# Optimization experiments

Hardware: AMD Instinct MI355X
Metric: run time of the kernel (lower is better)

The kernel has to match this reference:

```python
import jax, jax.numpy as jnp
import numpy as np

H, D, Kd, Vd = 16, 1024, 64, 64
N, Mlen = 4096, 4096


def setup_inputs() -> dict:
    key = jax.random.key(0)
    ks = jax.random.split(key, 7)
    X = jax.random.normal(ks[0], (N, D), dtype=jnp.float32)
    M = jax.random.normal(ks[1], (Mlen, D), dtype=jnp.float32)
    mask = jax.random.randint(ks[2], (N, Mlen), 0, 2, dtype=jnp.int32)
    Wq = jax.random.normal(ks[3], (H, D, Kd), dtype=jnp.float32)
    Wk = jax.random.normal(ks[4], (H, D, Kd), dtype=jnp.float32)
    Wv = jax.random.normal(ks[5], (H, D, Vd), dtype=jnp.float32)
    Wo = jax.random.normal(ks[6], (H, Vd, D), dtype=jnp.float32)
    return {"X": X, "M": M, "mask": mask, "Wq": Wq, "Wk": Wk, "Wv": Wv, "Wo": Wo}


def reference(X, M, mask, Wq, Wk, Wv, Wo):
    # Projections: [h,n,k], [h,m,k], [h,m,v]
    Q = jnp.einsum('nd,hdk->hnk', X, Wq)
    K = jnp.einsum('md,hdk->hmk', M, Wk)
    V = jnp.einsum('md,hdv->hmv', M, Wv)
    # Masked attention (no scaling, matching the source)
    logits = jnp.einsum('hnk,hmk->hnm', Q, K)
    logits = jnp.where(mask[None, :, :] == 0, -jnp.inf, logits)
    weights = jax.nn.softmax(logits, axis=-1)
    O = jnp.einsum('hnm,hmv->hnv', weights, V)
    Y = jnp.einsum('hnv,hvd->nd', O, Wo)
    return Y
```

## Files before the change

kernel.cpp:

```cpp
#include <hip/hip_runtime.h>

typedef _Float16 half8 __attribute__((ext_vector_type(8)));
typedef _Float16 half4 __attribute__((ext_vector_type(4)));
typedef __fp16 fp16x2 __attribute__((ext_vector_type(2)));
typedef short short8 __attribute__((ext_vector_type(8)));
typedef short short4v __attribute__((ext_vector_type(4)));
typedef float floatx4 __attribute__((ext_vector_type(4)));

#define LOG2E 1.4426950408889634f

#define GLDS16(g, l) __builtin_amdgcn_global_load_lds( \
    (const __attribute__((address_space(1))) unsigned int*)(g), \
    (__attribute__((address_space(3))) unsigned int*)(l), 16, 0, 0)

static __device__ __forceinline__ short f2bf(float f){
  union { float f; unsigned u; } v; v.f = f;
  unsigned r = v.u + 0x7fffu + ((v.u >> 16) & 1u);
  return (short)(r >> 16);
}
static __device__ __forceinline__ float bf2f(short s){
  union { unsigned u; float f; } v; v.u = ((unsigned)(unsigned short)s) << 16;
  return v.f;
}

__global__ __launch_bounds__(256) void kconvA(const float* __restrict__ X,
                                              const float* __restrict__ Mm,
                                              short* __restrict__ XFh, short* __restrict__ XFl,
                                              short* __restrict__ MFh, short* __restrict__ MFl){
  int b = blockIdx.x;
  int t = threadIdx.x, w = t >> 6, l = t & 63, quad = l >> 4;
  int srcsel = b >> 8, ntile = b & 255;
  const float* A = srcsel ? Mm : X;
  short* oh = srcsel ? MFh : XFh;
  short* ol = srcsel ? MFl : XFl;
  int row = ntile*16 + (l & 15);
  #pragma unroll
  for (int i = 0; i < 8; i++){
    int kt = w*8 + i;
    const float* p = A + (size_t)row*1024 + kt*32 + quad*8;
    float4 v0 = *(const float4*)p, v1 = *(const float4*)(p + 4);
    float vv[8] = {v0.x,v0.y,v0.z,v0.w,v1.x,v1.y,v1.z,v1.w};
    short8 hh, ll;
    #pragma unroll
    for (int j = 0; j < 8; j++){
      short hb = f2bf(vv[j]); hh[j] = hb; ll[j] = f2bf(vv[j] - bf2f(hb));
    }
    size_t off = ((size_t)kt*256 + ntile)*512 + l*8;
    *(short8*)&oh[off] = hh;
    *(short8*)&ol[off] = ll;
  }
}

__global__ __launch_bounds__(256) void kconvW2(const float* __restrict__ Wq,
                                               const float* __restrict__ Wk,
                                               const float* __restrict__ Wv,
                                               short* __restrict__ WFh, short* __restrict__ WFl){
  __shared__ float T[128][68];
  int bidx = blockIdx.x, g = blockIdx.y;
  int mat = bidx >> 4, h = bidx & 15;
  const float* W = (mat == 0 ? Wq : (mat == 1 ? Wk : Wv)) + (size_t)h*65536;
  int t = threadIdx.x, w = t >> 6, l = t & 63, quad = (l >> 4) & 3, fl = l & 15;
  #pragma unroll
  for (int p = 0; p < 32; p++){
    int idx = p*256 + t, row = idx >> 6, col = idx & 63;
    T[row][col] = W[(size_t)(g*128 + row)*64 + col];
  }
  __syncthreads();
  for (int ktl = 0; ktl < 4; ktl++){
    short8 hh, ll;
    #pragma unroll
    for (int j = 0; j < 8; j++){
      float v = T[ktl*32 + quad*8 + j][w*16 + fl];
      short hb = f2bf(v); hh[j] = hb; ll[j] = f2bf(v - bf2f(hb));
    }
    size_t frag = ((size_t)bidx*32 + g*4 + ktl)*4 + w;
    *(short8*)&WFh[frag*512 + l*8] = hh;
    *(short8*)&WFl[frag*512 + l*8] = ll;
  }
}

__global__ __launch_bounds__(256) void kmaskpack(const int* __restrict__ mask,
                                                 unsigned* __restrict__ bits){
  int w = blockIdx.x * 256 + threadIdx.x;
  const int* p = mask + (size_t)w * 32;
  unsigned b = 0;
  #pragma unroll
  for (int i = 0; i < 32; i++) b |= (p[i] != 0) ? (1u << i) : 0u;
  bits[w] = b;
}

__global__ __launch_bounds__(256) void ktransw(const float* __restrict__ src,
                                               short* __restrict__ dsth,
                                               short* __restrict__ dstl,
                                               int R, int C){
  __shared__ float tile[32][33];
  size_t boff = (size_t)blockIdx.z * R * C;
  src += boff; dsth += boff; dstl += boff;
  int r0 = blockIdx.y*32, c0 = blockIdx.x*32;
  int t = threadIdx.x, tr = t >> 3, tc = (t & 7)*4;
  const float* s = src + (size_t)(r0 + tr)*C + c0 + tc;
  #pragma unroll
  for (int i = 0; i < 4; i++) tile[tr][tc + i] = s[i];
  __syncthreads();
  short* dh = dsth + (size_t)(c0 + tr)*R + r0 + tc;
  short* dl = dstl + (size_t)(c0 + tr)*R + r0 + tc;
  #pragma unroll
  for (int i = 0; i < 4; i++){
    float v = tile[tc + i][tr];
    short hb = f2bf(v);
    dh[i] = hb; dl[i] = f2bf(v - bf2f(hb));
  }
}

__global__ __launch_bounds__(256,2) void kproj2(
    const short* __restrict__ XFh, const short* __restrict__ XFl,
    const short* __restrict__ MFh, const short* __restrict__ MFl,
    const short* __restrict__ WFh, const short* __restrict__ WFl,
    _Float16* __restrict__ QFh, _Float16* __restrict__ QFl,
    _Float16* __restrict__ KFh, _Float16* __restrict__ KFl,
    _Float16* __restrict__ VF)
{
  __shared__ short AhL[4096], AlL[4096], BhL[2048], BlL[2048];
  int cb = blockIdx.x, rb = blockIdx.y;
  int mat = cb >> 4, h = cb & 15;
  const short* Ah = (mat == 0) ? XFh : MFh;
  const short* Al = (mat == 0) ? XFl : MFl;
  int t = threadIdx.x, w = t >> 6, l = t & 63, quad = l >> 4, ln = l & 15;
  floatx4 acc[2][4] = {};
  for (int kt = 0; kt < 32; kt++){
    __syncthreads();
    size_t abase = ((size_t)kt*256 + rb*8)*512;
    #pragma unroll
    for (int i = 0; i < 2; i++){
      int cidx = i*256 + t;
      GLDS16(Ah + abase + cidx*8, &AhL[(i*256 + w*64)*8]);
      GLDS16(Al + abase + cidx*8, &AlL[(i*256 + w*64)*8]);
    }
    size_t bbase = (((size_t)cb*32 + kt)*4)*512;
    GLDS16(WFh + bbase + t*8, &BhL[(w*64)*8]);
    GLDS16(WFl + bbase + t*8, &BlL[(w*64)*8]);
    __syncthreads();
    short8 bh[4], bl[4];
    #pragma unroll
    for (int nt = 0; nt < 4; nt++){
      bh[nt] = *(short8*)&BhL[nt*512 + l*8];
      bl[nt] = *(short8*)&BlL[nt*512 + l*8];
    }
    #pragma unroll
    for (int mt = 0; mt < 2; mt++){
      short8 ah = *(short8*)&AhL[(w*2 + mt)*512 + l*8];
      short8 al = *(short8*)&AlL[(w*2 + mt)*512 + l*8];
      #pragma unroll
      for (int nt = 0; nt < 4; nt++){
        acc[mt][nt] = __builtin_amdgcn_mfma_f32_16x16x32_bf16(ah, bh[nt], acc[mt][nt], 0, 0, 0);
        acc[mt][nt] = __builtin_amdgcn_mfma_f32_16x16x32_bf16(ah, bl[nt], acc[mt][nt], 0, 0, 0);
        acc[mt][nt] = __builtin_amdgcn_mfma_f32_16x16x32_bf16(al, bh[nt], acc[mt][nt], 0, 0, 0);
      }
    }
  }
  int row0 = rb*128;
  if (mat == 2){
    #pragma unroll
    for (int mt = 0; mt < 2; mt++)
      #pragma unroll
      for (int nt = 0; nt < 4; nt++){
        union { fp16x2 h2[2]; unsigned u2[2]; } pu;
        pu.h2[0] = __builtin_amdgcn_cvt_pkrtz(acc[mt][nt][0], acc[mt][nt][1]);
        pu.h2[1] = __builtin_amdgcn_cvt_pkrtz(acc[mt][nt][2], acc[mt][nt][3]);
        size_t base = (((size_t)h*32 + rb)*16 + nt*4 + w)*512;
        *(uint2*)&VF[base + (quad*16 + ln)*8 + mt*4] = *(uint2*)&pu.u2[0];
      }
  } else {
    #pragma unroll
    for (int mt = 0; mt < 2; mt++)
      #pragma unroll
      for (int nt = 0; nt < 4; nt++)
        #pragma unroll
        for (int rg = 0; rg < 4; rg++){
          int n = row0 + w*32 + mt*16 + quad*4 + rg;
          int c = nt*16 + ln;
          float v = acc[mt][nt][rg];
          if (mat == 0) v *= LOG2E;
          _Float16 hi = (_Float16)v;
          _Float16 lo = (_Float16)(v - (float)hi);
          int lane2 = (n & 15) + (((c >> 3) & 3) << 4);
          size_t off = (((size_t)h*256 + (n >> 4))*2 + (c >> 5))*512 + lane2*8 + (c & 7);
          if (mat == 0){ QFh[off] = hi; QFl[off] = lo; }
          else         { KFh[off] = hi; KFl[off] = lo; }
        }
  }
}

__global__ __launch_bounds__(256,4) void kattn6(
    const _Float16* __restrict__ QFh, const _Float16* __restrict__ QFl,
    const _Float16* __restrict__ KFh, const _Float16* __restrict__ KFl,
    const _Float16* __restrict__ VF, const unsigned* __restrict__ bits,
    short* __restrict__ Ows)
{
  __shared__ _Float16 KBh[4096], KBl[4096], VB[4096];
  int bx = blockIdx.x, h = bx & 15, qb = bx >> 4, q0 = qb*64;
  int t = threadIdx.x, w = t >> 6, l = t & 63, quad = l >> 4, ln = l & 15;

  half8 qh[2], ql[2];
  #pragma unroll
  for (int kc = 0; kc < 2; kc++){
    size_t off = (((size_t)h*256 + qb*4 + w)*2 + kc)*512 + l*8;
    qh[kc] = *(const half8*)&QFh[off];
    ql[kc] = *(const half8*)&QFl[off];
  }

  floatx4 o[4] = {};
  float mst = -1e30f, lst = 0.f;

  for (int kt = 0; kt < 64; kt++){
    __syncthreads();
    size_t kb = (size_t)h*262144 + (size_t)kt*4096;
    size_t vb = (size_t)h*262144 + (size_t)(kt >> 1)*8192;
    int vhalf = (kt & 1)*2;
    #pragma unroll
    for (int i = 0; i < 2; i++){
      int cidx = i*256 + t;
      GLDS16(KFh + kb + cidx*8, &KBh[(i*256 + w*64)*8]);
      GLDS16(KFl + kb + cidx*8, &KBl[(i*256 + w*64)*8]);
      int lu = cidx >> 6, uoff = (cidx & 63)*8;
      int gu = (lu >> 1)*4 + vhalf + (lu & 1);
      GLDS16(VF + vb + (size_t)gu*512 + uoff, &VB[(i*256 + w*64)*8]);
    }
    uint2 mwv = *(const uint2*)&bits[(size_t)(q0 + w*16 + ln)*128 + kt*2];
    __syncthreads();

    floatx4 st[4] = {};
    #pragma unroll
    for (int kc = 0; kc < 2; kc++)
      #pragma unroll
      for (int m8 = 0; m8 < 4; m8++){
        half8 kh = *(half8*)&KBh[(m8*2 + kc)*512 + l*8];
        half8 kl = *(half8*)&KBl[(m8*2 + kc)*512 + l*8];
        st[m8] = __builtin_amdgcn_mfma_f32_16x16x32_f16(kh, qh[kc], st[m8], 0, 0, 0);
        st[m8] = __builtin_amdgcn_mfma_f32_16x16x32_f16(kl, qh[kc], st[m8], 0, 0, 0);
        st[m8] = __builtin_amdgcn_mfma_f32_16x16x32_f16(kh, ql[kc], st[m8], 0, 0, 0);
      }

    const unsigned mwp[2] = {mwv.x, mwv.y};
    #pragma unroll
    for (int m8 = 0; m8 < 4; m8++){
      unsigned nib = (mwp[m8 >> 1] >> ((m8 & 1)*16 + quad*4)) & 15u;
      #pragma unroll
      for (int rg = 0; rg < 4; rg++)
        if (!((nib >> rg) & 1u)) st[m8][rg] = -1e30f;
    }
    float mx = st[0][0];
    #pragma unroll
    for (int m8 = 0; m8 < 4; m8++)
      #pragma unroll
      for (int rg = 0; rg < 4; rg++) mx = fmaxf(mx, st[m8][rg]);
    mx = fmaxf(mx, __shfl_xor(mx, 16));
    mx = fmaxf(mx, __shfl_xor(mx, 32));
    float mnew = fmaxf(mst, mx);
    float alpha = exp2f(mst - mnew);
    mst = mnew;
    lst *= alpha;
    #pragma unroll
    for (int vt = 0; vt < 4; vt++) o[vt] *= alpha;
    float ssum = 0.f;
    #pragma unroll
    for (int m8 = 0; m8 < 4; m8++)
      #pragma unroll
      for (int rg = 0; rg < 4; rg++){
        float p = exp2f(st[m8][rg] - mnew);
        st[m8][rg] = p; ssum += p;
      }
    ssum += __shfl_xor(ssum, 16);
    ssum += __shfl_xor(ssum, 32);
    lst += ssum;

    #pragma unroll
    for (int p = 0; p < 2; p++){
      half8 vfp[4];
      #pragma unroll
      for (int vt = 0; vt < 4; vt++)
        vfp[vt] = *(half8*)&VB[((vt*2 + p)*512) + l*8];
      #pragma unroll
      for (int sub = 0; sub < 2; sub++){
        int m8 = p*2 + sub;
        union { fp16x2 h2[2]; half4 h4; } pu;
        pu.h2[0] = __builtin_amdgcn_cvt_pkrtz(st[m8][0], st[m8][1]);
        pu.h2[1] = __builtin_amdgcn_cvt_pkrtz(st[m8][2], st[m8][3]);
        #pragma unroll
        for (int vt = 0; vt < 4; vt++){
          half4 va = sub ? __builtin_shufflevector(vfp[vt], vfp[vt], 4,5,6,7)
                         : __builtin_shufflevector(vfp[vt], vfp[vt], 0,1,2,3);
          o[vt] = __builtin_amdgcn_mfma_f32_16x16x16f16(va, pu.h4, o[vt], 0, 0, 0);
        }
      }
    }
  }

  {
    float inv = (lst > 0.f) ? (1.f / lst) : 0.f;
    int n = q0 + w*16 + ln;
    #pragma unroll
    for (int vt = 0; vt < 4; vt++){
      short4v pk;
      #pragma unroll
      for (int rg = 0; rg < 4; rg++) pk[rg] = f2bf(o[vt][rg]*inv);
      *(short4v*)&Ows[(size_t)n*1024 + h*64 + vt*16 + quad*4] = pk;
    }
  }
}

__global__ __launch_bounds__(256,2) void kfinal(const short* __restrict__ Ain,
                                                const short* __restrict__ Bt,
                                                float* __restrict__ Y)
{
  __shared__ short Al[128*48];
  __shared__ short Bl[64*48];
  int cb = blockIdx.x, rb = blockIdx.y;
  int row0 = rb*128, col0 = cb*64;
  int t = threadIdx.x, w = t >> 6, l = t & 63, quad = l >> 4, ln = l & 15;
  floatx4 acc[2][4] = {};
  for (int d0 = 0; d0 < 1024; d0 += 32){
    #pragma unroll
    for (int i = 0; i < 2; i++){
      int u = t + i*256, r = u >> 2, s = u & 3;
      *(int4*)&Al[r*48 + s*8] = *(const int4*)&Ain[(size_t)(row0 + r)*1024 + d0 + s*8];
    }
    { int r = t >> 2, s = t & 3;
      *(int4*)&Bl[r*48 + s*8] = *(const int4*)&Bt[(size_t)(col0 + r)*1024 + d0 + s*8]; }
    __syncthreads();
    short8 bf[4];
    #pragma unroll
    for (int nt = 0; nt < 4; nt++) bf[nt] = *(short8*)&Bl[(nt*16 + ln)*48 + quad*8];
    #pragma unroll
    for (int mt = 0; mt < 2; mt++){
      short8 af = *(short8*)&Al[(w*32 + mt*16 + ln)*48 + quad*8];
      #pragma unroll
      for (int nt = 0; nt < 4; nt++)
        acc[mt][nt] = __builtin_amdgcn_mfma_f32_16x16x32_bf16(af, bf[nt], acc[mt][nt], 0, 0, 0);
    }
    __syncthreads();
  }
  #pragma unroll
  for (int mt = 0; mt < 2; mt++)
    #pragma unroll
    for (int nt = 0; nt < 4; nt++)
      #pragma unroll
      for (int rg = 0; rg < 4; rg++){
        int n = row0 + w*32 + mt*16 + quad*4 + rg;
        int c = col0 + nt*16 + ln;
        Y[(size_t)n*1024 + c] = acc[mt][nt][rg];
      }
}

extern "C" void kernel_launch(void* const* d_in, const int* in_sizes, int n_in,
                              void* d_out, int out_size, void* d_ws, size_t ws_size,
                              hipStream_t stream){
  (void)in_sizes; (void)n_in; (void)out_size; (void)ws_size;
  const float* X    = (const float*)d_in[0];
  const float* Mm   = (const float*)d_in[1];
  const int*   mask = (const int*)d_in[2];
  const float* Wq   = (const float*)d_in[3];
  const float* Wk   = (const float*)d_in[4];
  const float* Wv   = (const float*)d_in[5];
  const float* Wo   = (const float*)d_in[6];
  float* Y = (float*)d_out;
  char* ws = (char*)d_ws;
  const size_t MB = 1024*1024;
  short*    XFh   = (short*)   (ws +  0*MB);
  short*    XFl   = (short*)   (ws +  8*MB);
  short*    MFh   = (short*)   (ws + 16*MB);
  short*    MFl   = (short*)   (ws + 24*MB);
  short*    WFh   = (short*)   (ws + 32*MB);
  short*    WFl   = (short*)   (ws + 38*MB);
  unsigned* bits  = (unsigned*)(ws + 44*MB);
  _Float16* QFh   = (_Float16*)(ws + 46*MB);
  _Float16* QFl   = (_Float16*)(ws + 54*MB);
  _Float16* KFh   = (_Float16*)(ws + 62*MB);
  _Float16* KFl   = (_Float16*)(ws + 70*MB);
  _Float16* VF    = (_Float16*)(ws + 78*MB);
  short*    Ows   = (short*)   (ws +  0*MB);
  short*    Wot   = (short*)   (ws +  8*MB);
  short*    Wotl  = (short*)   (ws + 10*MB);

  kconvA<<<512, 256, 0, stream>>>(X, Mm, XFh, XFl, MFh, MFl);
  kconvW2<<<dim3(48,8), 256, 0, stream>>>(Wq, Wk, Wv, WFh, WFl);
  kmaskpack<<<2048, 256, 0, stream>>>(mask, bits);
  kproj2<<<dim3(48,32), 256, 0, stream>>>(XFh, XFl, MFh, MFl, WFh, WFl,
                                          QFh, QFl, KFh, KFl, VF);
  ktransw<<<dim3(32,32,1), 256, 0, stream>>>(Wo, Wot, Wotl, 1024, 1024);
  kattn6<<<1024, 256, 0, stream>>>(QFh, QFl, KFh, KFl, VF, bits, Ows);
  kfinal<<<dim3(16,32), 256, 0, stream>>>(Ows, Wot, Y);
}
```

Before: 493.6 us.

## Double-buffer K tiles, prefetch V and mask, and skip small rescales

Splits the K shared-memory buffers into two and issues the next tile's K loads and mask-word load before the current tile's QK MFMAs. The V tile is now reloaded after the PV product rather than at the top of the loop, which replaces the stall-prone load-then-sync pattern with overlapped transfers. It also unrolls the row max into a tree and only rescales the running max and accumulators when the new max exceeds the old one by more than 8. That lazy rescaling trades exact max tracking for fewer exp and multiply operations, and risks overflow or accuracy loss when values grow within the threshold. It also uses more LDS per block, which may lower occupancy.

```diff
diff --git a/kernel.cpp b/kernel.cpp
--- a/kernel.cpp
+++ b/kernel.cpp
@@ -191,13 +191,13 @@
   }
 }
 
-__global__ __launch_bounds__(256,4) void kattn6(
+__global__ __launch_bounds__(256,4) void kattn7(
     const _Float16* __restrict__ QFh, const _Float16* __restrict__ QFl,
     const _Float16* __restrict__ KFh, const _Float16* __restrict__ KFl,
     const _Float16* __restrict__ VF, const unsigned* __restrict__ bits,
     short* __restrict__ Ows)
 {
-  __shared__ _Float16 KBh[4096], KBl[4096], VB[4096];
+  __shared__ _Float16 KBh[2][4096], KBl[2][4096], VB[4096];
   int bx = blockIdx.x, h = bx & 15, qb = bx >> 4, q0 = qb*64;
   int t = threadIdx.x, w = t >> 6, l = t & 63, quad = l >> 4, ln = l & 15;
 
@@ -212,67 +212,87 @@
   floatx4 o[4] = {};
   float mst = -1e30f, lst = 0.f;
 
-  for (int kt = 0; kt < 64; kt++){
-    __syncthreads();
-    size_t kb = (size_t)h*262144 + (size_t)kt*4096;
-    size_t vb = (size_t)h*262144 + (size_t)(kt >> 1)*8192;
-    int vhalf = (kt & 1)*2;
+  const size_t hb = (size_t)h*262144;
+  const int cidx0 = t, cidx1 = 256 + t;
+  const int ld0 = (w*64)*8, ld1 = (256 + w*64)*8;
+
+  {
+    GLDS16(KFh + hb + cidx0*8, &KBh[0][ld0]);
+    GLDS16(KFh + hb + cidx1*8, &KBh[0][ld1]);
+    GLDS16(KFl + hb + cidx0*8, &KBl[0][ld0]);
+    GLDS16(KFl + hb + cidx1*8, &KBl[0][ld1]);
     #pragma unroll
     for (int i = 0; i < 2; i++){
       int cidx = i*256 + t;
-      GLDS16(KFh + kb + cidx*8, &KBh[(i*256 + w*64)*8]);
-      GLDS16(KFl + kb + cidx*8, &KBl[(i*256 + w*64)*8]);
       int lu = cidx >> 6, uoff = (cidx & 63)*8;
-      int gu = (lu >> 1)*4 + vhalf + (lu & 1);
-      GLDS16(VF + vb + (size_t)gu*512 + uoff, &VB[(i*256 + w*64)*8]);
-    }
-    uint2 mwv = *(const uint2*)&bits[(size_t)(q0 + w*16 + ln)*128 + kt*2];
-    __syncthreads();
+      int gu = (lu >> 1)*4 + (lu & 1);
+      GLDS16(VF + hb + (size_t)gu*512 + uoff, &VB[(i*256 + w*64)*8]);
+    }
+  }
+  uint2 mwv = *(const uint2*)&bits[(size_t)(q0 + w*16 + ln)*128];
+  __syncthreads();
+
+  int cur = 0;
+  for (int kt = 0; kt < 64; kt++){
+    int ktn = (kt + 1) & 63;
+    size_t kbn = hb + (size_t)ktn*4096;
+    GLDS16(KFh + kbn + cidx0*8, &KBh[cur^1][ld0]);
+    GLDS16(KFh + kbn + cidx1*8, &KBh[cur^1][ld1]);
+    GLDS16(KFl + kbn + cidx0*8, &KBl[cur^1][ld0]);
+    GLDS16(KFl + kbn + cidx1*8, &KBl[cur^1][ld1]);
+    uint2 mwn = *(const uint2*)&bits[(size_t)(q0 + w*16 + ln)*128 + ktn*2];
 
     floatx4 st[4] = {};
     #pragma unroll
     for (int kc = 0; kc < 2; kc++)
       #pragma unroll
       for (int m8 = 0; m8 < 4; m8++){
-        half8 kh = *(half8*)&KBh[(m8*2 + kc)*512 + l*8];
-        half8 kl = *(half8*)&KBl[(m8*2 + kc)*512 + l*8];
+        half8 kh = *(half8*)&KBh[cur][(m8*2 + kc)*512 + l*8];
+        half8 kl = *(half8*)&KBl[cur][(m8*2 + kc)*512 + l*8];
         st[m8] = __builtin_amdgcn_mfma_f32_16x16x32_f16(kh, qh[kc], st[m8], 0, 0, 0);
         st[m8] = __builtin_amdgcn_mfma_f32_16x16x32_f16(kl, qh[kc], st[m8], 0, 0, 0);
         st[m8] = __builtin_amdgcn_mfma_f32_16x16x32_f16(kh, ql[kc], st[m8], 0, 0, 0);
       }
 
-    const unsigned mwp[2] = {mwv.x, mwv.y};
-    #pragma unroll
-    for (int m8 = 0; m8 < 4; m8++){
-      unsigned nib = (mwp[m8 >> 1] >> ((m8 & 1)*16 + quad*4)) & 15u;
-      #pragma unroll
-      for (int rg = 0; rg < 4; rg++)
-        if (!((nib >> rg) & 1u)) st[m8][rg] = -1e30f;
-    }
-    float mx = st[0][0];
-    #pragma unroll
-    for (int m8 = 0; m8 < 4; m8++)
-      #pragma unroll
-      for (int rg = 0; rg < 4; rg++) mx = fmaxf(mx, st[m8][rg]);
-    mx = fmaxf(mx, __shfl_xor(mx, 16));
-    mx = fmaxf(mx, __shfl_xor(mx, 32));
-    float mnew = fmaxf(mst, mx);
-    float alpha = exp2f(mst - mnew);
-    mst = mnew;
-    lst *= alpha;
-    #pragma unroll
-    for (int vt = 0; vt < 4; vt++) o[vt] *= alpha;
-    float ssum = 0.f;
-    #pragma unroll
-    for (int m8 = 0; m8 < 4; m8++)
-      #pragma unroll
-      for (int rg = 0; rg < 4; rg++){
-        float p = exp2f(st[m8][rg] - mnew);
-        st[m8][rg] = p; ssum += p;
-      }
-    ssum += __shfl_xor(ssum, 16);
-    ssum += __shfl_xor(ssum, 32);
-    lst += ssum;
+    {
+      const unsigned mwp[2] = {mwv.x, mwv.y};
+      #pragma unroll
+      for (int m8 = 0; m8 < 4; m8++){
+        unsigned nib = (mwp[m8 >> 1] >> ((m8 & 1)*16 + quad*4)) & 15u;
+        #pragma unroll
+        for (int rg = 0; rg < 4; rg++)
+          if (!((nib >> rg) & 1u)) st[m8][rg] = -1e30f;
+      }
+      float a0 = fmaxf(fmaxf(st[0][0], st[0][1]), fmaxf(st[0][2], st[0][3]));
+      float a1 = fmaxf(fmaxf(st[1][0], st[1][1]), fmaxf(st[1][2], st[1][3]));
+      float a2 = fmaxf(fmaxf(st[2][0], st[2][1]), fmaxf(st[2][2], st[2][3]));
+      float a3 = fmaxf(fmaxf(st[3][0], st[3][1]), fmaxf(st[3][2], st[3][3]));
+      float mx = fmaxf(fmaxf(a0, a1), fmaxf(a2, a3));
+      mx = fmaxf(mx, __shfl_xor(mx, 16));
+      mx = fmaxf(mx, __shfl_xor(mx, 32));
+      if (__any(mx > mst + 8.0f)){
+        float mnew = fmaxf(mst, mx);
+        float alpha = exp2f(mst - mnew);
+        mst = mnew;
+        lst *= alpha;
+        #pragma unroll
+        for (int vt = 0; vt < 4; vt++) o[vt] *= alpha;
+      }
+      float ssum = 0.f;
+      #pragma unroll
+      for (int m8 = 0; m8 < 4; m8++)
+        #pragma unroll
+        for (int rg = 0; rg < 4; rg++){
+          float p = exp2f(st[m8][rg] - mst);
+          st[m8][rg] = p; ssum += p;
+        }
+      ssum += __shfl_xor(ssum, 16);
+      ssum += __shfl_xor(ssum, 32);
+      lst += ssum;
+    }
+    mwv = mwn;
+
+    __syncthreads();
 
     #pragma unroll
     for (int p = 0; p < 2; p++){
@@ -294,6 +314,21 @@
         }
       }
     }
+
+    __syncthreads();
+
+    {
+      size_t vbn = hb + (size_t)(ktn >> 1)*8192;
+      int vhalf = (ktn & 1)*2;
+      #pragma unroll
+      for (int i = 0; i < 2; i++){
+        int cidx = i*256 + t;
+        int lu = cidx >> 6, uoff = (cidx & 63)*8;
+        int gu = (lu >> 1)*4 + vhalf + (lu & 1);
+        GLDS16(VF + vbn + (size_t)gu*512 + uoff, &VB[(i*256 + w*64)*8]);
+      }
+    }
+    cur ^= 1;
   }
 
   {
@@ -388,6 +423,6 @@
   kproj2<<<dim3(48,32), 256, 0, stream>>>(XFh, XFl, MFh, MFl, WFh, WFl,
                                           QFh, QFl, KFh, KFl, VF);
   ktransw<<<dim3(32,32,1), 256, 0, stream>>>(Wo, Wot, Wotl, 1024, 1024);
-  kattn6<<<1024, 256, 0, stream>>>(QFh, QFl, KFh, KFl, VF, bits, Ows);
+  kattn7<<<1024, 256, 0, stream>>>(QFh, QFl, KFh, KFl, VF, bits, Ows);
   kfinal<<<dim3(16,32), 256, 0, stream>>>(Ows, Wot, Y);
 }
```

Measured after the change: 489.2 us. About the same (-0.9%).
